# Kernel tuning notes

Hardware: AMD Instinct MI355X
Metric: run time of the kernel (lower is better)

Reference implementation:

```python
import jax, jax.numpy as jnp
import numpy as np

N, E, D_IN, HID, OUT, H = 20000, 320000, 128, 128, 128, 4

def _lin(key, fan_in, fan_out):
    kw, kb = jax.random.split(key)
    W = jax.random.normal(kw, (fan_in, fan_out), jnp.float32) * 0.05
    b = jax.random.normal(kb, (fan_out,), jnp.float32) * 0.05
    return W, b

def setup_inputs() -> dict:
    key = jax.random.key(0)
    ks = jax.random.split(key, 10)
    x = jax.random.normal(ks[0], (N, D_IN), jnp.float32)
    edge_index = jax.random.randint(ks[1], (2, E), 0, N, jnp.int32)
    # Layer 0: TransformerConv(D_IN -> HID, heads=H, concat=True)
    Wq0, bq0 = _lin(ks[2], D_IN, H * HID)
    Wk0, bk0 = _lin(ks[3], D_IN, H * HID)
    Wv0, bv0 = _lin(ks[4], D_IN, H * HID)
    Ws0, bs0 = _lin(ks[5], D_IN, H * HID)   # root/skip projection
    # Layer 1: TransformerConv(H*HID -> OUT, heads=H, concat=False)
    Wq1, bq1 = _lin(ks[6], H * HID, H * OUT)
    Wk1, bk1 = _lin(ks[7], H * HID, H * OUT)
    Wv1, bv1 = _lin(ks[8], H * HID, H * OUT)
    Ws1, bs1 = _lin(ks[9], H * HID, OUT)    # skip maps to OUT when concat=False
    return dict(x=x, edge_index=edge_index,
                Wq0=Wq0, bq0=bq0, Wk0=Wk0, bk0=bk0, Wv0=Wv0, bv0=bv0, Ws0=Ws0, bs0=bs0,
                Wq1=Wq1, bq1=bq1, Wk1=Wk1, bk1=bk1, Wv1=Wv1, bv1=bv1, Ws1=Ws1, bs1=bs1)

def _transformer_conv(x, src, dst, Wq, bq, Wk, bk, Wv, bv, Ws, bs, heads, out_ch, concat):
    n = x.shape[0]
    q = (x @ Wq + bq).reshape(n, heads, out_ch)
    k = (x @ Wk + bk).reshape(n, heads, out_ch)
    v = (x @ Wv + bv).reshape(n, heads, out_ch)
    # per-edge attention logits: [E, H]
    alpha = jnp.einsum('ehc,ehc->eh', q[dst], k[src]) / jnp.sqrt(jnp.float32(out_ch))
    # softmax grouped by destination node (numerically stable)
    m = jax.ops.segment_max(alpha, dst, num_segments=n)        # [N, H]
    alpha = jnp.exp(alpha - m[dst])
    s = jax.ops.segment_sum(alpha, dst, num_segments=n)       # [N, H]
    alpha = alpha / (s[dst] + 1e-16)
    # weighted scatter-add of messages: [N, H, C]
    out = jax.ops.segment_sum(alpha[..., None] * v[src], dst, num_segments=n)
    if concat:
        out = out.reshape(n, heads * out_ch)
    else:
        out = out.mean(axis=1)
    return out + x @ Ws + bs  # root weight (skip connection)

def reference(x, edge_index,
              Wq0, bq0, Wk0, bk0, Wv0, bv0, Ws0, bs0,
              Wq1, bq1, Wk1, bk1, Wv1, bv1, Ws1, bs1):
    src, dst = edge_index[0], edge_index[1]
    h = _transformer_conv(x, src, dst, Wq0, bq0, Wk0, bk0, Wv0, bv0, Ws0, bs0, H, HID, True)
    h = jax.nn.relu(h)  # dropout is identity in eval mode
    out = _transformer_conv(h, src, dst, Wq1, bq1, Wk1, bk1, Wv1, bv1, Ws1, bs1, H, OUT, False)
    return out
```

## Files before the change

### kernel.cpp

```cpp
#include <hip/hip_runtime.h>
#include <hip/hip_bf16.h>
#include <math.h>

#define HCH    512
#define OUTD   128
#define N0CAT  2048
#define N1CAT  1664
#define P0STR  1024
#define P1STR  640
#define KVW    1024
#define DCAP   64

typedef __attribute__((ext_vector_type(8))) short short8v;
typedef __attribute__((ext_vector_type(8))) unsigned short ushort8v;
typedef __attribute__((ext_vector_type(4))) unsigned short ushort4v;
typedef __attribute__((ext_vector_type(4))) float floatx4;
typedef __attribute__((ext_vector_type(2))) float floatx2;
typedef __attribute__((ext_vector_type(4))) unsigned int uintx4;

__device__ inline float bf2f(unsigned short u) {
    return __uint_as_float(((unsigned)u) << 16);
}

__device__ inline unsigned short f2bf(float f) {
    return (unsigned short)__bfloat16_as_ushort(__float2bfloat16(f));
}

template <bool HI>
__device__ inline floatx2 fp8x2_to_f32(unsigned int w) {
    return __builtin_amdgcn_cvt_pk_f32_fp8(w, HI);
}

__device__ inline unsigned int f32x4_to_fp8(float a, float b, float c, float d) {
    int w = __builtin_amdgcn_cvt_pk_fp8_f32(a, b, 0, false);
    w = __builtin_amdgcn_cvt_pk_fp8_f32(c, d, w, true);
    return (unsigned int)w;
}

__device__ inline void gload_lds16(const void* g, void* l) {
    __builtin_amdgcn_global_load_lds(
        (const __attribute__((address_space(1))) unsigned int*)g,
        (__attribute__((address_space(3))) unsigned int*)l, 16, 0, 0);
}


__global__ void bucket_kernel(const int* __restrict__ src, const int* __restrict__ dst,
                              int* __restrict__ deg, int* __restrict__ srcs, int E) {
    int e = blockIdx.x * 256 + threadIdx.x;
    if (e < E) {
        int d = dst[e];
        int pos = atomicAdd(&deg[d], 1);
        if (pos < DCAP) srcs[d * DCAP + pos] = src[e];
    }
}


__device__ void tpose_tile(const float* __restrict__ W, __hip_bfloat16* __restrict__ o,
                           int K, int C, int bx, int by, int t, float (*tile)[33]) {
    int c0 = bx * 32, k0 = by * 32;
    int tx = t & 31, ty = t >> 5;
    #pragma unroll
    for (int r = ty; r < 32; r += 8)
        tile[r][tx] = W[(size_t)(k0 + r) * C + c0 + tx];
    __syncthreads();
    #pragma unroll
    for (int r = ty; r < 32; r += 8)
        o[(size_t)(c0 + r) * K + k0 + tx] = __float2bfloat16(tile[tx][r]);
}

__global__ __launch_bounds__(256) void prep_all(
        const float* __restrict__ x, __hip_bfloat16* __restrict__ Xb,
        const float* __restrict__ Wq0, const float* __restrict__ Wk0,
        const float* __restrict__ Wv0, const float* __restrict__ Ws0,
        const float* __restrict__ Wq1, const float* __restrict__ Wk1,
        const float* __restrict__ Wv1, const float* __restrict__ Ws1,
        const float* __restrict__ bq0, const float* __restrict__ bk0,
        const float* __restrict__ bv0, const float* __restrict__ bs0,
        const float* __restrict__ bq1, const float* __restrict__ bk1,
        const float* __restrict__ bv1, const float* __restrict__ bs1,
        __hip_bfloat16* __restrict__ Wc0, __hip_bfloat16* __restrict__ Wc1,
        float* __restrict__ bc0, float* __restrict__ bc1,
        int* __restrict__ deg, int N) {
    __shared__ float tile[32][33];
    int t = threadIdx.x;
    int b = blockIdx.x;
    int nb_cast = (N * 128 + 255) >> 8;
    if (b < nb_cast) {
        int i = b * 256 + t;
        if (i < N * 128) Xb[i] = __float2bfloat16(x[i]);
        return;
    }
    b -= nb_cast;
    if (b < 256) {
        int z = b >> 6, rem = b & 63;
        const float* W = (z == 0) ? Wq0 : (z == 1) ? Wk0 : (z == 2) ? Wv0 : Ws0;
        tpose_tile(W, Wc0 + (size_t)z * 512 * 128, 128, 512, rem & 15, rem >> 4, t, tile);
        return;
    }
    b -= 256;
    if (b < 768) {
        int z = b >> 8, rem = b & 255;
        const float* W = (z == 0) ? Wq1 : (z == 1) ? Wk1 : Wv1;
        tpose_tile(W, Wc1 + (size_t)z * 512 * 512, 512, 512, rem & 15, rem >> 4, t, tile);
        return;
    }
    b -= 768;
    if (b < 64) {
        tpose_tile(Ws1, Wc1 + (size_t)1536 * 512, 512, 128, b & 3, b >> 2, t, tile);
        return;
    }
    b -= 64;
    if (b < 8) {
        int i = b * 256 + t;
        if (i < N0CAT) {
            int sel = i >> 9, col = i & 511;
            const float* bb = (sel == 0) ? bq0 : (sel == 1) ? bk0 : (sel == 2) ? bv0 : bs0;
            bc0[i] = bb[col];
        }
        if (i < N1CAT) {
            if (i < 1536) {
                int sel = i >> 9, col = i & 511;
                const float* bb = (sel == 0) ? bq1 : (sel == 1) ? bk1 : bv1;
                bc1[i] = bb[col];
            } else {
                bc1[i] = bs1[i - 1536];
            }
        }
        return;
    }
    b -= 8;
    {
        int i = b * 256 + t;
        if (i < N) deg[i] = 0;
    }
}


#define BM 128
#define BN 128
#define BK 64

__global__ __launch_bounds__(256) void gemm_mfma(const __hip_bfloat16* __restrict__ A,
                                                 const __hip_bfloat16* __restrict__ Bt,
                                                 const float* __restrict__ bias,
                                                 __hip_bfloat16* __restrict__ P,
                                                 int pstride,
                                                 unsigned char* __restrict__ KV8,
                                                 int M, int K, int Nd, int mt_pad) {
    __shared__ __hip_bfloat16 As[BM][BK];
    __shared__ __hip_bfloat16 Bs[BN][BK];
    int f = blockIdx.x;
    int mt = f % mt_pad, nt = f / mt_pad;
    int bm = mt * BM, bn = nt * BN;
    if (bm >= M) return;
    int t = threadIdx.x;
    int lane = t & 63, w = t >> 6;
    int quad = lane >> 4, l16 = lane & 15;
    int wm = (w >> 1) * 64, wn = (w & 1) * 64;

    int srow = w * 8 + (lane >> 3);
    int c8g = (lane & 7) ^ ((lane >> 3) & 7);
    const char* Ab = (const char*)(A + (size_t)(bm + srow) * K + c8g * 8);
    const char* Bb = (const char*)(Bt + (size_t)(bn + srow) * K + c8g * 8);
    char* Al = (char*)&As[0][0] + w * 1024;
    char* Bl = (char*)&Bs[0][0] + w * 1024;

    int sw = l16 & 7;

    floatx4 acc[4][4];
    #pragma unroll
    for (int i = 0; i < 4; i++)
        #pragma unroll
        for (int j = 0; j < 4; j++)
            acc[i][j] = (floatx4)0.0f;

    for (int k0 = 0; k0 < K; k0 += BK) {
        __syncthreads();
        #pragma unroll
        for (int i = 0; i < 4; i++) {
            size_t go = ((size_t)i * 32 * K + k0) * 2;
            gload_lds16(Ab + go, Al + i * 4096);
            gload_lds16(Bb + go, Bl + i * 4096);
        }
        __syncthreads();
        #pragma unroll
        for (int ks = 0; ks < BK; ks += 32) {
            int c8a = (quad + (ks >> 3)) ^ sw;
            short8v af[4], bfr[4];
            #pragma unroll
            for (int i = 0; i < 4; i++)
                af[i] = *(const short8v*)&As[wm + i * 16 + l16][c8a * 8];
            #pragma unroll
            for (int j = 0; j < 4; j++)
                bfr[j] = *(const short8v*)&Bs[wn + j * 16 + l16][c8a * 8];
            #pragma unroll
            for (int i = 0; i < 4; i++)
                #pragma unroll
                for (int j = 0; j < 4; j++)
                    acc[i][j] = __builtin_amdgcn_mfma_f32_16x16x32_bf16(bfr[j], af[i], acc[i][j], 0, 0, 0);
        }
    }

    #pragma unroll
    for (int i = 0; i < 4; i++) {
        int row = bm + wm + i * 16 + l16;
        if (row >= M) continue;
        #pragma unroll
        for (int j = 0; j < 4; j++) {
            int col = bn + wn + j * 16 + quad * 4;
            floatx4 bv = *(const floatx4*)(bias + col);
            float v0 = acc[i][j][0] + bv[0];
            float v1 = acc[i][j][1] + bv[1];
            float v2 = acc[i][j][2] + bv[2];
            float v3 = acc[i][j][3] + bv[3];
            if (col < 512) {
                ushort4v o = { f2bf(v0), f2bf(v1), f2bf(v2), f2bf(v3) };
                *(ushort4v*)(P + (size_t)row * pstride + col) = o;
            } else if (col < 1024) {
                int b = col - 512;
                int nb = ((b >> 3) << 4) + (b & 7);
                *(unsigned int*)(KV8 + (size_t)row * KVW + nb) = f32x4_to_fp8(v0, v1, v2, v3);
            } else if (col < 1536) {
                int b = col - 1024;
                int nb = ((b >> 3) << 4) + 8 + (b & 7);
                *(unsigned int*)(KV8 + (size_t)row * KVW + nb) = f32x4_to_fp8(v0, v1, v2, v3);
            } else {
                ushort4v o = { f2bf(v0), f2bf(v1), f2bf(v2), f2bf(v3) };
                *(ushort4v*)(P + (size_t)row * pstride + 512 + (col - 1536)) = o;
            }
        }
    }
}


#define PF 4

__global__ __launch_bounds__(256) void attn_kernel(const __hip_bfloat16* __restrict__ P,
                                                   int pstride,
                                                   const unsigned char* __restrict__ KV8,
                                                   const int* __restrict__ deg,
                                                   const int* __restrict__ srcs,
                                                   __hip_bfloat16* __restrict__ out_b,
                                                   float* __restrict__ out_f,
                                                   int n_nodes, int mode) {
    int wave = threadIdx.x >> 6;
    int lane = threadIdx.x & 63;
    int node = blockIdx.x * 4 + wave;
    if (node >= n_nodes) return;
    const float scale = 0.08838834764831845f;

    const __hip_bfloat16* Prow = P + (size_t)node * pstride;
    float qf[8];
    {
        ushort8v qu = *(const ushort8v*)(Prow + lane * 8);
        #pragma unroll
        for (int j = 0; j < 8; j++) qf[j] = bf2f(qu[j]) * scale;
    }

    float l = 0.f;
    float acc[8] = {0.f, 0.f, 0.f, 0.f, 0.f, 0.f, 0.f, 0.f};

    int cnt = deg[node];
    if (cnt > DCAP) cnt = DCAP;
    const int* ep = srcs + (size_t)node * DCAP;
    const unsigned char* Kb = KV8 + lane * 16;

    uintx4 kv[PF];
    #pragma unroll
    for (int i = 0; i < PF; i++) {
        if (i < cnt) {
            int s = ep[i];
            kv[i] = *(const uintx4*)(Kb + (size_t)s * KVW);
        }
    }

    int e = 0;
    for (; e + PF <= cnt; e += PF) {
        #pragma unroll
        for (int i = 0; i < PF; i++) {
            uintx4 u = kv[i];
            int pe = e + i + PF;
            if (pe < cnt) {
                int s = ep[pe];
                kv[i] = *(const uintx4*)(Kb + (size_t)s * KVW);
            }
            floatx2 k01 = fp8x2_to_f32<false>(u[0]);
            floatx2 k23 = fp8x2_to_f32<true >(u[0]);
            floatx2 k45 = fp8x2_to_f32<false>(u[1]);
            floatx2 k67 = fp8x2_to_f32<true >(u[1]);
            float part = qf[0] * k01[0] + qf[1] * k01[1]
                       + qf[2] * k23[0] + qf[3] * k23[1]
                       + qf[4] * k45[0] + qf[5] * k45[1]
                       + qf[6] * k67[0] + qf[7] * k67[1];
            part += __shfl_xor(part, 1);
            part += __shfl_xor(part, 2);
            part += __shfl_xor(part, 4);
            part += __shfl_xor(part, 8);
            float p = __expf(part);
            l += p;
            floatx2 v01 = fp8x2_to_f32<false>(u[2]);
            floatx2 v23 = fp8x2_to_f32<true >(u[2]);
            floatx2 v45 = fp8x2_to_f32<false>(u[3]);
            floatx2 v67 = fp8x2_to_f32<true >(u[3]);
            acc[0] += p * v01[0];
            acc[1] += p * v01[1];
            acc[2] += p * v23[0];
            acc[3] += p * v23[1];
            acc[4] += p * v45[0];
            acc[5] += p * v45[1];
            acc[6] += p * v67[0];
            acc[7] += p * v67[1];
        }
    }
    #pragma unroll
    for (int i = 0; i < PF; i++) {
        if (e + i < cnt) {
            uintx4 u = kv[i];
            floatx2 k01 = fp8x2_to_f32<false>(u[0]);
            floatx2 k23 = fp8x2_to_f32<true >(u[0]);
            floatx2 k45 = fp8x2_to_f32<false>(u[1]);
            floatx2 k67 = fp8x2_to_f32<true >(u[1]);
            float part = qf[0] * k01[0] + qf[1] * k01[1]
                       + qf[2] * k23[0] + qf[3] * k23[1]
                       + qf[4] * k45[0] + qf[5] * k45[1]
                       + qf[6] * k67[0] + qf[7] * k67[1];
            part += __shfl_xor(part, 1);
            part += __shfl_xor(part, 2);
            part += __shfl_xor(part, 4);
            part += __shfl_xor(part, 8);
            float p = __expf(part);
            l += p;
            floatx2 v01 = fp8x2_to_f32<false>(u[2]);
            floatx2 v23 = fp8x2_to_f32<true >(u[2]);
            floatx2 v45 = fp8x2_to_f32<false>(u[3]);
            floatx2 v67 = fp8x2_to_f32<true >(u[3]);
            acc[0] += p * v01[0];
            acc[1] += p * v01[1];
            acc[2] += p * v23[0];
            acc[3] += p * v23[1];
            acc[4] += p * v45[0];
            acc[5] += p * v45[1];
            acc[6] += p * v67[0];
            acc[7] += p * v67[1];
        }
    }
    float inv = (l > 0.f) ? 1.f / l : 0.f;

    if (mode == 0) {
        ushort8v su = *(const ushort8v*)(Prow + 512 + lane * 8);
        ushort8v o;
        #pragma unroll
        for (int j = 0; j < 8; j++) {
            float r = fmaxf(acc[j] * inv + bf2f(su[j]), 0.f);
            o[j] = f2bf(r);
        }
        *(ushort8v*)(out_b + (size_t)node * HCH + lane * 8) = o;
    } else {
        float r[8];
        #pragma unroll
        for (int j = 0; j < 8; j++) {
            r[j] = acc[j] * inv;
            r[j] += __shfl_xor(r[j], 16);
            r[j] += __shfl_xor(r[j], 32);
            r[j] *= 0.25f;
        }
        if (lane < 16) {
            const __hip_bfloat16* sp = Prow + 512 + lane * 8;
            float* op = out_f + (size_t)node * OUTD + lane * 8;
            #pragma unroll
            for (int j = 0; j < 8; j++) op[j] = r[j] + bf2f(__bfloat16_as_ushort(sp[j]));
        }
    }
}


static inline size_t align256(size_t x) { return (x + 255) & ~(size_t)255; }

extern "C" void kernel_launch(void* const* d_in, const int* in_sizes, int n_in,
                              void* d_out, int out_size, void* d_ws, size_t ws_size,
                              hipStream_t stream) {
    const float* x   = (const float*)d_in[0];
    const int*   ei  = (const int*)d_in[1];
    const float* Wq0 = (const float*)d_in[2];  const float* bq0 = (const float*)d_in[3];
    const float* Wk0 = (const float*)d_in[4];  const float* bk0 = (const float*)d_in[5];
    const float* Wv0 = (const float*)d_in[6];  const float* bv0 = (const float*)d_in[7];
    const float* Ws0 = (const float*)d_in[8];  const float* bs0 = (const float*)d_in[9];
    const float* Wq1 = (const float*)d_in[10]; const float* bq1 = (const float*)d_in[11];
    const float* Wk1 = (const float*)d_in[12]; const float* bk1 = (const float*)d_in[13];
    const float* Wv1 = (const float*)d_in[14]; const float* bv1 = (const float*)d_in[15];
    const float* Ws1 = (const float*)d_in[16]; const float* bs1 = (const float*)d_in[17];
    float* out = (float*)d_out;

    const int N = in_sizes[0] / 128;
    const int E = in_sizes[1] / 2;
    const int* src = ei;
    const int* dst = ei + E;

    int mtiles = (N + BM - 1) / BM;
    int mt_pad = (mtiles + 7) & ~7;
    const int Mpad = mt_pad * BM;

    char* ws = (char*)d_ws;
    __hip_bfloat16* P0  = (__hip_bfloat16*)ws; ws += align256((size_t)N * P0STR * 2);
    __hip_bfloat16* P1  = P0;
    __hip_bfloat16* Hbb = (__hip_bfloat16*)ws; ws += align256((size_t)Mpad * HCH * 2);
    __hip_bfloat16* Xb  = (__hip_bfloat16*)ws; ws += align256((size_t)Mpad * 128 * 2);
    unsigned char* KV8  = (unsigned char*)ws;  ws += align256((size_t)N * KVW);
    __hip_bfloat16* Wc0 = (__hip_bfloat16*)ws; ws += align256((size_t)N0CAT * 128 * 2);
    __hip_bfloat16* Wc1 = (__hip_bfloat16*)ws; ws += align256((size_t)N1CAT * 512 * 2);
    float* bc0 = (float*)ws; ws += align256((size_t)N0CAT * 4);
    float* bc1 = (float*)ws; ws += align256((size_t)N1CAT * 4);
    int* deg    = (int*)ws; ws += align256((size_t)N * 4);
    int* srcs   = (int*)ws; ws += align256((size_t)N * DCAP * 4);

    dim3 blk(256);

    int nb_cast = (N * 128 + 255) / 256;
    int nb_deg = (N + 255) / 256;
    int nb_prep = nb_cast + 256 + 768 + 64 + 8 + nb_deg;
    prep_all<<<nb_prep, blk, 0, stream>>>(
        x, Xb, Wq0, Wk0, Wv0, Ws0, Wq1, Wk1, Wv1, Ws1,
        bq0, bk0, bv0, bs0, bq1, bk1, bv1, bs1,
        Wc0, Wc1, bc0, bc1, deg, N);

    bucket_kernel<<<(E + 255) / 256, 256, 0, stream>>>(src, dst, deg, srcs, E);

    gemm_mfma<<<dim3(mt_pad * (N0CAT / BN)), blk, 0, stream>>>(
        Xb, Wc0, bc0, P0, P0STR, KV8, N, 128, N0CAT, mt_pad);
    attn_kernel<<<(N + 3) / 4, blk, 0, stream>>>(P0, P0STR, KV8, deg, srcs, Hbb, nullptr, N, 0);

    gemm_mfma<<<dim3(mt_pad * (N1CAT / BN)), blk, 0, stream>>>(
        Hbb, Wc1, bc1, P1, P1STR, KV8, N, 512, N1CAT, mt_pad);
    attn_kernel<<<(N + 3) / 4, blk, 0, stream>>>(P1, P1STR, KV8, deg, srcs, nullptr, out, N, 1);
}
```

Measured before the change: 328.4 us.

## Double-buffer GEMM LDS tiles, fold edge bucketing into prep, use packed math in attention

The GEMM now keeps two LDS buffers and issues the next K-tile's global-to-LDS loads before computing the current one, with explicit vmcnt waits, barriers and raised wave priority around the MFMA block. The edge-bucketing pass moves into the prep kernel, and the degree array is cleared with a memset, which removes one kernel launch. The attention kernel uses two-wide float vectors for the dot product and accumulation and folds log2(e) into the query scale so it can call exp2. Doubling LDS per block may reduce occupancy, and the hand-written vmcnt counts must match the number of loads actually issued.

```diff
diff --git a/kernel.cpp b/kernel.cpp
--- a/kernel.cpp
+++ b/kernel.cpp
@@ -41,17 +41,6 @@
     __builtin_amdgcn_global_load_lds(
         (const __attribute__((address_space(1))) unsigned int*)g,
         (__attribute__((address_space(3))) unsigned int*)l, 16, 0, 0);
-}
-
-
-__global__ void bucket_kernel(const int* __restrict__ src, const int* __restrict__ dst,
-                              int* __restrict__ deg, int* __restrict__ srcs, int E) {
-    int e = blockIdx.x * 256 + threadIdx.x;
-    if (e < E) {
-        int d = dst[e];
-        int pos = atomicAdd(&deg[d], 1);
-        if (pos < DCAP) srcs[d * DCAP + pos] = src[e];
-    }
 }
 
 
@@ -80,7 +69,9 @@
         const float* __restrict__ bv1, const float* __restrict__ bs1,
         __hip_bfloat16* __restrict__ Wc0, __hip_bfloat16* __restrict__ Wc1,
         float* __restrict__ bc0, float* __restrict__ bc1,
-        int* __restrict__ deg, int N) {
+        int* __restrict__ deg, int* __restrict__ srcs,
+        const int* __restrict__ srce, const int* __restrict__ dste,
+        int N, int E) {
     __shared__ float tile[32][33];
     int t = threadIdx.x;
     int b = blockIdx.x;
@@ -130,8 +121,12 @@
     }
     b -= 8;
     {
-        int i = b * 256 + t;
-        if (i < N) deg[i] = 0;
+        int e = b * 256 + t;
+        if (e < E) {
+            int d = dste[e];
+            int pos = atomicAdd(&deg[d], 1);
+            if (pos < DCAP) srcs[d * DCAP + pos] = srce[e];
+        }
     }
 }
 
@@ -139,6 +134,7 @@
 #define BM 128
 #define BN 128
 #define BK 64
+#define TILEB (BM * BK * 2)
 
 __global__ __launch_bounds__(256) void gemm_mfma(const __hip_bfloat16* __restrict__ A,
                                                  const __hip_bfloat16* __restrict__ Bt,
@@ -147,8 +143,8 @@
                                                  int pstride,
                                                  unsigned char* __restrict__ KV8,
                                                  int M, int K, int Nd, int mt_pad) {
-    __shared__ __hip_bfloat16 As[BM][BK];
-    __shared__ __hip_bfloat16 Bs[BN][BK];
+    __shared__ __hip_bfloat16 As[2][BM][BK];
+    __shared__ __hip_bfloat16 Bs[2][BN][BK];
     int f = blockIdx.x;
     int mt = f % mt_pad, nt = f / mt_pad;
     int bm = mt * BM, bn = nt * BN;
@@ -162,8 +158,8 @@
     int c8g = (lane & 7) ^ ((lane >> 3) & 7);
     const char* Ab = (const char*)(A + (size_t)(bm + srow) * K + c8g * 8);
     const char* Bb = (const char*)(Bt + (size_t)(bn + srow) * K + c8g * 8);
-    char* Al = (char*)&As[0][0] + w * 1024;
-    char* Bl = (char*)&Bs[0][0] + w * 1024;
+    char* Al = (char*)&As[0][0][0] + w * 1024;
+    char* Bl = (char*)&Bs[0][0][0] + w * 1024;
 
     int sw = l16 & 7;
 
@@ -174,31 +170,48 @@
         for (int j = 0; j < 4; j++)
             acc[i][j] = (floatx4)0.0f;
 
-    for (int k0 = 0; k0 < K; k0 += BK) {
-        __syncthreads();
+    auto issue_tile = [&](int k0, int bsel) {
         #pragma unroll
         for (int i = 0; i < 4; i++) {
             size_t go = ((size_t)i * 32 * K + k0) * 2;
-            gload_lds16(Ab + go, Al + i * 4096);
-            gload_lds16(Bb + go, Bl + i * 4096);
-        }
-        __syncthreads();
+            gload_lds16(Ab + go, Al + bsel * TILEB + i * 4096);
+            gload_lds16(Bb + go, Bl + bsel * TILEB + i * 4096);
+        }
+    };
+
+    issue_tile(0, 0);
+    int nk = K / BK;
+    for (int tt = 0; tt < nk; tt++) {
+        int cur = tt & 1;
+        if (tt + 1 < nk) {
+            issue_tile((tt + 1) * BK, cur ^ 1);
+            asm volatile("s_waitcnt vmcnt(8)" ::: "memory");
+        } else {
+            asm volatile("s_waitcnt vmcnt(0)" ::: "memory");
+        }
+        __builtin_amdgcn_s_barrier();
+        __builtin_amdgcn_sched_barrier(0);
+        __builtin_amdgcn_s_setprio(1);
         #pragma unroll
         for (int ks = 0; ks < BK; ks += 32) {
             int c8a = (quad + (ks >> 3)) ^ sw;
             short8v af[4], bfr[4];
             #pragma unroll
             for (int i = 0; i < 4; i++)
-                af[i] = *(const short8v*)&As[wm + i * 16 + l16][c8a * 8];
+                af[i] = *(const short8v*)&As[cur][wm + i * 16 + l16][c8a * 8];
             #pragma unroll
             for (int j = 0; j < 4; j++)
-                bfr[j] = *(const short8v*)&Bs[wn + j * 16 + l16][c8a * 8];
+                bfr[j] = *(const short8v*)&Bs[cur][wn + j * 16 + l16][c8a * 8];
             #pragma unroll
             for (int i = 0; i < 4; i++)
                 #pragma unroll
                 for (int j = 0; j < 4; j++)
                     acc[i][j] = __builtin_amdgcn_mfma_f32_16x16x32_bf16(bfr[j], af[i], acc[i][j], 0, 0, 0);
         }
+        __builtin_amdgcn_s_setprio(0);
+        __builtin_amdgcn_sched_barrier(0);
+        __builtin_amdgcn_s_barrier();
+        __builtin_amdgcn_sched_barrier(0);
     }
 
     #pragma unroll
@@ -247,18 +260,23 @@
     int lane = threadIdx.x & 63;
     int node = blockIdx.x * 4 + wave;
     if (node >= n_nodes) return;
-    const float scale = 0.08838834764831845f;
+    const float qsc = 0.08838834764831845f * 1.4426950408889634f;
 
     const __hip_bfloat16* Prow = P + (size_t)node * pstride;
-    float qf[8];
+    floatx2 q2[4];
     {
         ushort8v qu = *(const ushort8v*)(Prow + lane * 8);
         #pragma unroll
-        for (int j = 0; j < 8; j++) qf[j] = bf2f(qu[j]) * scale;
+        for (int j = 0; j < 4; j++) {
+            q2[j][0] = bf2f(qu[2 * j])     * qsc;
+            q2[j][1] = bf2f(qu[2 * j + 1]) * qsc;
+        }
     }
 
     float l = 0.f;
-    float acc[8] = {0.f, 0.f, 0.f, 0.f, 0.f, 0.f, 0.f, 0.f};
+    floatx2 acc2[4];
+    #pragma unroll
+    for (int j = 0; j < 4; j++) acc2[j] = (floatx2)0.0f;
 
     int cnt = deg[node];
     if (cnt > DCAP) cnt = DCAP;
@@ -288,28 +306,26 @@
             floatx2 k23 = fp8x2_to_f32<true >(u[0]);
             floatx2 k45 = fp8x2_to_f32<false>(u[1]);
             floatx2 k67 = fp8x2_to_f32<true >(u[1]);
-            float part = qf[0] * k01[0] + qf[1] * k01[1]
-                       + qf[2] * k23[0] + qf[3] * k23[1]
-                       + qf[4] * k45[0] + qf[5] * k45[1]
-                       + qf[6] * k67[0] + qf[7] * k67[1];
+            floatx2 d2 = q2[0] * k01;
+            d2 += q2[1] * k23;
+            d2 += q2[2] * k45;
+            d2 += q2[3] * k67;
+            float part = d2[0] + d2[1];
             part += __shfl_xor(part, 1);
             part += __shfl_xor(part, 2);
             part += __shfl_xor(part, 4);
             part += __shfl_xor(part, 8);
-            float p = __expf(part);
+            float p = exp2f(part);
             l += p;
+            floatx2 pv = { p, p };
             floatx2 v01 = fp8x2_to_f32<false>(u[2]);
             floatx2 v23 = fp8x2_to_f32<true >(u[2]);
             floatx2 v45 = fp8x2_to_f32<false>(u[3]);
             floatx2 v67 = fp8x2_to_f32<true >(u[3]);
-            acc[0] += p * v01[0];
-            acc[1] += p * v01[1];
-            acc[2] += p * v23[0];
-            acc[3] += p * v23[1];
-            acc[4] += p * v45[0];
-            acc[5] += p * v45[1];
-            acc[6] += p * v67[0];
-            acc[7] += p * v67[1];
+            acc2[0] += pv * v01;
+            acc2[1] += pv * v23;
+            acc2[2] += pv * v45;
+            acc2[3] += pv * v67;
         }
     }
     #pragma unroll
@@ -320,28 +336,26 @@
             floatx2 k23 = fp8x2_to_f32<true >(u[0]);
             floatx2 k45 = fp8x2_to_f32<false>(u[1]);
             floatx2 k67 = fp8x2_to_f32<true >(u[1]);
-            float part = qf[0] * k01[0] + qf[1] * k01[1]
-                       + qf[2] * k23[0] + qf[3] * k23[1]
-                       + qf[4] * k45[0] + qf[5] * k45[1]
-                       + qf[6] * k67[0] + qf[7] * k67[1];
+            floatx2 d2 = q2[0] * k01;
+            d2 += q2[1] * k23;
+            d2 += q2[2] * k45;
+            d2 += q2[3] * k67;
+            float part = d2[0] + d2[1];
             part += __shfl_xor(part, 1);
             part += __shfl_xor(part, 2);
             part += __shfl_xor(part, 4);
             part += __shfl_xor(part, 8);
-            float p = __expf(part);
+            float p = exp2f(part);
             l += p;
+            floatx2 pv = { p, p };
             floatx2 v01 = fp8x2_to_f32<false>(u[2]);
             floatx2 v23 = fp8x2_to_f32<true >(u[2]);
             floatx2 v45 = fp8x2_to_f32<false>(u[3]);
             floatx2 v67 = fp8x2_to_f32<true >(u[3]);
-            acc[0] += p * v01[0];
-            acc[1] += p * v01[1];
-            acc[2] += p * v23[0];
-            acc[3] += p * v23[1];
-            acc[4] += p * v45[0];
-            acc[5] += p * v45[1];
-            acc[6] += p * v67[0];
-            acc[7] += p * v67[1];
+            acc2[0] += pv * v01;
+            acc2[1] += pv * v23;
+            acc2[2] += pv * v45;
+            acc2[3] += pv * v67;
         }
     }
     float inv = (l > 0.f) ? 1.f / l : 0.f;
@@ -351,7 +365,7 @@
         ushort8v o;
         #pragma unroll
         for (int j = 0; j < 8; j++) {
-            float r = fmaxf(acc[j] * inv + bf2f(su[j]), 0.f);
+            float r = fmaxf(acc2[j >> 1][j & 1] * inv + bf2f(su[j]), 0.f);
             o[j] = f2bf(r);
         }
         *(ushort8v*)(out_b + (size_t)node * HCH + lane * 8) = o;
@@ -359,7 +373,7 @@
         float r[8];
         #pragma unroll
         for (int j = 0; j < 8; j++) {
-            r[j] = acc[j] * inv;
+            r[j] = acc2[j >> 1][j & 1] * inv;
             r[j] += __shfl_xor(r[j], 16);
             r[j] += __shfl_xor(r[j], 32);
             r[j] *= 0.25f;
@@ -415,15 +429,15 @@
 
     dim3 blk(256);
 
+    hipMemsetAsync(deg, 0, (size_t)N * 4, stream);
+
     int nb_cast = (N * 128 + 255) / 256;
-    int nb_deg = (N + 255) / 256;
-    int nb_prep = nb_cast + 256 + 768 + 64 + 8 + nb_deg;
+    int nb_bucket = (E + 255) / 256;
+    int nb_prep = nb_cast + 256 + 768 + 64 + 8 + nb_bucket;
     prep_all<<<nb_prep, blk, 0, stream>>>(
         x, Xb, Wq0, Wk0, Wv0, Ws0, Wq1, Wk1, Wv1, Ws1,
         bq0, bk0, bv0, bs0, bq1, bk1, bv1, bs1,
-        Wc0, Wc1, bc0, bc1, deg, N);
-
-    bucket_kernel<<<(E + 255) / 256, 256, 0, stream>>>(src, dst, deg, srcs, E);
+        Wc0, Wc1, bc0, bc1, deg, srcs, src, dst, N, E);
 
     gemm_mfma<<<dim3(mt_pad * (N0CAT / BN)), blk, 0, stream>>>(
         Xb, Wc0, bc0, P0, P0STR, KV8, N, 128, N0CAT, mt_pad);
```

New measurement: 332.1 us. About the same (+1.1%).
